# Kernel optimization log

Hardware: AMD Instinct MI355X
Metric: run time of the kernel (lower is better)

## Reference

```python
import jax, jax.numpy as jnp
import numpy as np
from jax import lax

B, T = 16, 64
SD, LD, C, K, A = 256, 256, 32, 32, 6   # state_dim, latent_dim, num_categories, num_classes, action_dim
FS = SD + C * K                          # full_state_dim = 1280
KL_BETA, KL_BAL = 1.0, 0.8


def _conv(x, w, b):  # stride-2, k4, pad1 conv (torch Conv2d(k=4,s=2,p=1))
    y = lax.conv_general_dilated(x, w, (2, 2), ((1, 1), (1, 1)),
                                 dimension_numbers=('NCHW', 'OIHW', 'NCHW'))
    return y + b[None, :, None, None]


def _convT(x, w, b):  # stride-2 VALID conv-transpose: out = (in-1)*2 + k
    y = lax.conv_transpose(x, w, (2, 2), 'VALID',
                           dimension_numbers=('NCHW', 'OIHW', 'NCHW'))
    return y + b[None, :, None, None]


def setup_inputs() -> dict:
    key = jax.random.key(0)
    ks = iter(jax.random.split(key, 64))
    def rn(shape, s=0.05):
        return jax.random.normal(next(ks), shape, jnp.float32) * s
    def zb(n):
        return jnp.zeros((n,), jnp.float32)
    inp = dict(
        observations=jax.random.uniform(next(ks), (B, T + 1, 3, 64, 64), jnp.float32),
        actions=jax.random.randint(next(ks), (B, T), 0, A, dtype=jnp.int32),
        rewards=jax.random.normal(next(ks), (B, T), jnp.float32),
        # encoder: 3->32->64->128->256, then 256*4*4 -> latent_dim
        ew1=rn((32, 3, 4, 4)), eb1=zb(32), ew2=rn((64, 32, 4, 4)), eb2=zb(64),
        ew3=rn((128, 64, 4, 4)), eb3=zb(128), ew4=rn((256, 128, 4, 4)), eb4=zb(256),
        enc_lw=rn((4096, LD)), enc_lb=zb(LD),
        # rssm
        pre_w=rn((C * K + A, SD)), pre_b=zb(SD),
        gru_wi=rn((SD, 3 * SD)), gru_wh=rn((SD, 3 * SD)), gru_bi=zb(3 * SD), gru_bh=zb(3 * SD),
        pri_w1=rn((SD, 256)), pri_b1=zb(256), pri_w2=rn((256, C * K)), pri_b2=zb(C * K),
        post_w1=rn((SD + LD, 256)), post_b1=zb(256), post_w2=rn((256, C * K)), post_b2=zb(C * K),
        # decoder: 1280 -> 1024 -> (1024,1,1) -> 3x64x64
        dec_lw=rn((FS, 1024)), dec_lb=zb(1024),
        dw1=rn((128, 1024, 5, 5)), db1=zb(128), dw2=rn((64, 128, 5, 5)), db2=zb(64),
        dw3=rn((32, 64, 6, 6)), db3=zb(32), dw4=rn((3, 32, 6, 6)), db4=zb(3),
        # reward head
        rw1=rn((FS, 256)), rb1=zb(256), rw2=rn((256, 1)), rb2=zb(1),
        # fixed gumbel noise for straight-through categorical sampling (T,B,C,K)
        gumbel=-jnp.log(-jnp.log(jax.random.uniform(next(ks), (T, B, C, K), jnp.float32, 1e-6, 1.0 - 1e-6))),
    )
    return inp


def reference(observations, actions, rewards,
              ew1, eb1, ew2, eb2, ew3, eb3, ew4, eb4, enc_lw, enc_lb,
              pre_w, pre_b, gru_wi, gru_wh, gru_bi, gru_bh,
              pri_w1, pri_b1, pri_w2, pri_b2, post_w1, post_b1, post_w2, post_b2,
              dec_lw, dec_lb, dw1, db1, dw2, db2, dw3, db3, dw4, db4,
              rw1, rb1, rw2, rb2, gumbel):
    relu, sg = jax.nn.relu, lax.stop_gradient
    b, tp1 = observations.shape[:2]
    t = tp1 - 1

    # ---- encoder over all frames ----
    x = observations.reshape(-1, 3, 64, 64)
    x = relu(_conv(x, ew1, eb1))
    x = relu(_conv(x, ew2, eb2))
    x = relu(_conv(x, ew3, eb3))
    x = relu(_conv(x, ew4, eb4))                      # (B*(T+1), 256, 4, 4)
    embeds = (x.reshape(x.shape[0], -1) @ enc_lw + enc_lb).reshape(b, tp1, LD)

    a_oh = jax.nn.one_hot(actions, A, dtype=jnp.float32).transpose(1, 0, 2)  # (T,B,A)
    emb_t = embeds[:, 1:].transpose(1, 0, 2)                                 # (T,B,LD)

    h0 = jnp.zeros((b, SD), jnp.float32)
    s0 = jnp.zeros((b, C * K), jnp.float32)

    def step(carry, inp):
        h, stoch = carry
        a, e, g = inp
        xin = relu(jnp.concatenate([stoch, a], -1) @ pre_w + pre_b)
        # GRU cell
        gi = xin @ gru_wi + gru_bi
        gh = h @ gru_wh + gru_bh
        ir, iz, inn = jnp.split(gi, 3, -1)
        hr, hz, hn = jnp.split(gh, 3, -1)
        r = jax.nn.sigmoid(ir + hr)
        z = jax.nn.sigmoid(iz + hz)
        n = jnp.tanh(inn + r * hn)
        h = (1.0 - z) * n + z * h
        prior = (relu(h @ pri_w1 + pri_b1) @ pri_w2 + pri_b2).reshape(b, C, K)
        post = (relu(jnp.concatenate([h, e], -1) @ post_w1 + post_b1) @ post_w2 + post_b2).reshape(b, C, K)
        # straight-through categorical sample from posterior
        idx = jnp.argmax(post + g, -1)
        probs = jax.nn.softmax(post, -1)
        sample = jax.nn.one_hot(idx, K, dtype=jnp.float32) + probs - sg(probs)
        stoch = sample.reshape(b, C * K)
        full = jnp.concatenate([h, stoch], -1)
        return (h, stoch), (prior, post, full)

    _, (priors, posts, fulls) = lax.scan(step, (h0, s0), (a_oh, emb_t, gumbel))
    priors = priors.transpose(1, 0, 2, 3)             # (B,T,C,K)
    posts = posts.transpose(1, 0, 2, 3)
    fulls = fulls.transpose(1, 0, 2).reshape(b * t, FS)

    # ---- decoder ----
    d = (fulls @ dec_lw + dec_lb).reshape(-1, 1024, 1, 1)
    d = relu(_convT(d, dw1, db1))                     # (.,128,5,5)
    d = relu(_convT(d, dw2, db2))                     # (.,64,13,13)
    d = relu(_convT(d, dw3, db3))                     # (.,32,30,30)
    recon = _convT(d, dw4, db4).reshape(b, t, 3, 64, 64)

    reward_pred = (relu(fulls @ rw1 + rb1) @ rw2 + rb2).reshape(b, t)

    recon_loss = jnp.mean((recon - observations[:, 1:]) ** 2)
    reward_loss = jnp.mean((reward_pred - rewards) ** 2)

    pp = jax.nn.softmax(posts, -1) + 1e-8
    qp = jax.nn.softmax(priors, -1) + 1e-8
    pl = jnp.log(pp)
    ql = jnp.log(qp)
    kl = (KL_BAL * jnp.mean(jnp.sum(sg(pp) * (sg(pl) - ql), -1))
          + (1.0 - KL_BAL) * jnp.mean(jnp.sum(pp * (pl - sg(ql)), -1)))

    return recon_loss + reward_loss + KL_BETA * kl
```

## Files before the change

### kernel.cpp

```cpp
#include <hip/hip_runtime.h>
#include <math.h>

#define DI __device__ __forceinline__

constexpr int TB = 16, TT = 64, NF = 1040, FSD = 1280;
constexpr int CHF = 208;
constexpr int CHN = 256;

constexpr size_t OFF_X1C  = 0;
constexpr size_t OFF_X2C  = 6815744;
constexpr size_t OFF_X3C  = 10223616;
constexpr size_t OFF_D0T  = 0;
constexpr size_t OFF_DD1  = 262144;
constexpr size_t OFF_DD2  = 1081344;
constexpr size_t OFF_DD3  = 3850240;
constexpr size_t OFF_X4   = 11927552;
constexpr size_t OFF_W1T  = 11927552;
constexpr size_t OFF_W2T  = 15204352;
constexpr size_t OFF_W3T  = 15409152;
constexpr size_t OFF_W4P  = 15482880;
constexpr size_t OFF_EMB  = 16187392;
constexpr size_t OFF_FULL = 16453632;
constexpr size_t OFF_PRI  = 17764352;
constexpr size_t OFF_POS  = 18812928;
constexpr size_t OFF_H    = 19861504;
constexpr size_t OFF_GI   = 19865600;
constexpr size_t OFF_GH   = 19877888;
constexpr size_t OFF_Q1   = 19890176;
constexpr size_t OFF_CIDX = 19894272;
constexpr size_t OFF_BARS = 19894784;
constexpr size_t OFF_ACC  = 19895296;
constexpr size_t WS_NEED_BYTES = (OFF_ACC + 16) * 4;

__global__ void k_init(int* bars, double* accs) {
  int i = threadIdx.x;
  if (i < 512) bars[i] = 0;
  if (i < 4) accs[i] = 0.0;
}

__global__ void __launch_bounds__(256) k_conv1(const float* __restrict__ obs,
    const float* __restrict__ w, const float* __restrict__ b, float* __restrict__ out, int fb) {
  __shared__ float in_s[3*66*66];
  __shared__ float w_s[32*48];
  const int f = blockIdx.x, tid = threadIdx.x;
  const float* src = obs + (size_t)(fb + f)*12288;
  for (int i = tid; i < 3*66*66; i += 256) {
    int c = i/4356, p = i%4356, y = p/66, x = p%66;
    float v = 0.f;
    if (y >= 1 && y <= 64 && x >= 1 && x <= 64) v = src[(c<<12) + ((y-1)<<6) + (x-1)];
    in_s[i] = v;
  }
  for (int i = tid; i < 32*48; i += 256) w_s[i] = w[i];
  __syncthreads();
  for (int pp = 0; pp < 4; ++pp) {
    int pos = tid + pp*256;
    int y = pos >> 5, x = pos & 31;
    float tp[48];
    #pragma unroll
    for (int c = 0; c < 3; ++c)
      #pragma unroll
      for (int ky = 0; ky < 4; ++ky)
        #pragma unroll
        for (int kx = 0; kx < 4; ++kx)
          tp[c*16+ky*4+kx] = in_s[c*4356 + (2*y+ky)*66 + (2*x+kx)];
    for (int o = 0; o < 32; ++o) {
      float acc = b[o];
      #pragma unroll
      for (int t = 0; t < 48; ++t) acc += tp[t]*w_s[o*48+t];
      out[((size_t)f*32 + o)*1024 + pos] = fmaxf(acc, 0.f);
    }
  }
}

__global__ void __launch_bounds__(256) k_conv2(const float* __restrict__ in,
    const float* __restrict__ w, const float* __restrict__ bias, float* __restrict__ out) {
  __shared__ float in_s[8*34*34];
  __shared__ float w_s[32*128];
  const int f = blockIdx.x, oh = blockIdx.y, tid = threadIdx.x;
  const int y = tid >> 4, x = tid & 15;
  float acc[32];
  #pragma unroll
  for (int o = 0; o < 32; ++o) acc[o] = bias[oh*32 + o];
  for (int cc = 0; cc < 4; ++cc) {
    __syncthreads();
    for (int i = tid; i < 8*34*34; i += 256) {
      int c = i/1156, p = i%1156, yy = p/34, xx = p%34;
      float v = 0.f;
      if (yy >= 1 && yy <= 32 && xx >= 1 && xx <= 32)
        v = in[((size_t)f*32 + cc*8 + c)*1024 + ((yy-1)<<5) + (xx-1)];
      in_s[i] = v;
    }
    for (int i = tid; i < 4096; i += 256) {
      int o = i >> 7, r = i & 127;
      w_s[i] = w[(oh*32+o)*512 + cc*128 + r];
    }
    __syncthreads();
    #pragma unroll
    for (int c = 0; c < 8; ++c) {
      float tp[16];
      #pragma unroll
      for (int ky = 0; ky < 4; ++ky)
        #pragma unroll
        for (int kx = 0; kx < 4; ++kx)
          tp[ky*4+kx] = in_s[c*1156 + (2*y+ky)*34 + (2*x+kx)];
      #pragma unroll
      for (int o = 0; o < 32; ++o) {
        float a2 = acc[o];
        #pragma unroll
        for (int t = 0; t < 16; ++t) a2 += tp[t]*w_s[(o<<7) + (c<<4) + t];
        acc[o] = a2;
      }
    }
  }
  #pragma unroll
  for (int o = 0; o < 32; ++o)
    out[((size_t)f*64 + oh*32 + o)*256 + tid] = fmaxf(acc[o], 0.f);
}

__global__ void __launch_bounds__(256) k_conv3(const float* __restrict__ in,
    const float* __restrict__ w, const float* __restrict__ bias, float* __restrict__ out) {
  __shared__ float in_s[4*18*18];
  __shared__ float w_s[128*64];
  const int f = blockIdx.x, tid = threadIdx.x;
  const int pos = tid & 63, cog = tid >> 6;
  const int y = pos >> 3, x = pos & 7;
  float acc[32];
  #pragma unroll
  for (int o = 0; o < 32; ++o) acc[o] = bias[cog*32+o];
  for (int cc = 0; cc < 16; ++cc) {
    __syncthreads();
    for (int i = tid; i < 1296; i += 256) {
      int c = i/324, p = i%324, yy = p/18, xx = p%18;
      float v = 0.f;
      if (yy >= 1 && yy <= 16 && xx >= 1 && xx <= 16)
        v = in[((size_t)f*64 + cc*4 + c)*256 + ((yy-1)<<4) + (xx-1)];
      in_s[i] = v;
    }
    for (int i = tid; i < 8192; i += 256) {
      int o = i >> 6, r = i & 63;
      w_s[i] = w[o*1024 + cc*64 + r];
    }
    __syncthreads();
    #pragma unroll
    for (int c = 0; c < 4; ++c) {
      float tp[16];
      #pragma unroll
      for (int ky = 0; ky < 4; ++ky)
        #pragma unroll
        for (int kx = 0; kx < 4; ++kx)
          tp[ky*4+kx] = in_s[c*324 + (2*y+ky)*18 + (2*x+kx)];
      #pragma unroll
      for (int o = 0; o < 32; ++o) {
        float a2 = acc[o];
        #pragma unroll
        for (int t = 0; t < 16; ++t) a2 += tp[t]*w_s[((cog*32+o)<<6) + (c<<4) + t];
        acc[o] = a2;
      }
    }
  }
  #pragma unroll
  for (int o = 0; o < 32; ++o)
    out[((size_t)f*128 + cog*32 + o)*64 + pos] = fmaxf(acc[o], 0.f);
}

__global__ void __launch_bounds__(256) k_conv4(const float* __restrict__ in,
    const float* __restrict__ w, const float* __restrict__ bias, float* __restrict__ out, int fb) {
  __shared__ float a_s[32*256];
  __shared__ float w_s[64*32];
  const int f0 = blockIdx.x * 16, o0 = blockIdx.y * 64, tid = threadIdx.x;
  const int fl = tid >> 4, pos = tid & 15;
  float acc[64];
  #pragma unroll
  for (int o = 0; o < 64; ++o) acc[o] = 0.f;
  for (int K0 = 0; K0 < 2048; K0 += 32) {
    __syncthreads();
    for (int i = tid; i < 8192; i += 256) {
      int kk = i >> 8, row = i & 255;
      int K = K0 + kk, ci = K >> 4, tap = K & 15;
      int ff = f0 + (row >> 4), pp = row & 15;
      int yy = ((pp >> 2) << 1) + (tap >> 2) - 1;
      int xx = ((pp & 3) << 1) + (tap & 3) - 1;
      float v = 0.f;
      if (yy >= 0 && yy < 8 && xx >= 0 && xx < 8)
        v = in[((size_t)ff*128 + ci)*64 + yy*8 + xx];
      a_s[kk*256 + row] = v;
    }
    for (int i = tid; i < 2048; i += 256) {
      int o = i >> 5, kk = i & 31;
      w_s[i] = w[(o0 + o)*2048 + K0 + kk];
    }
    __syncthreads();
    #pragma unroll
    for (int kk = 0; kk < 32; ++kk) {
      float av = a_s[kk*256 + tid];
      #pragma unroll
      for (int o = 0; o < 64; ++o) acc[o] += av * w_s[o*32 + kk];
    }
  }
  for (int o = 0; o < 64; ++o)
    out[(((size_t)(fb + f0 + fl))*256 + o0+o)*16 + pos] = fmaxf(acc[o] + bias[o0+o], 0.f);
}

__global__ void __launch_bounds__(256) k_enclin(const float* __restrict__ x4,
    const float* __restrict__ w, const float* __restrict__ b, float* __restrict__ emb) {
  __shared__ float a_s[4*1024];
  const int f0 = blockIdx.x*4, tid = threadIdx.x;
  float acc[4] = {0.f,0.f,0.f,0.f};
  for (int K0 = 0; K0 < 4096; K0 += 1024) {
    __syncthreads();
    for (int i = tid; i < 4096; i += 256) {
      int r = i >> 10, k = i & 1023;
      a_s[i] = x4[((size_t)(f0+r))*4096 + K0 + k];
    }
    __syncthreads();
    for (int k = 0; k < 1024; ++k) {
      float wv = w[(K0+k)*256 + tid];
      #pragma unroll
      for (int r = 0; r < 4; ++r) acc[r] += a_s[(r<<10) + k] * wv;
    }
  }
  #pragma unroll
  for (int r = 0; r < 4; ++r) emb[((size_t)(f0+r))*256 + tid] = acc[r] + b[tid];
}

__global__ void k_wtrans(const float* __restrict__ dw1, const float* __restrict__ dw2,
                         const float* __restrict__ dw3, const float* __restrict__ dw4,
                         float* __restrict__ w1t, float* __restrict__ w2t,
                         float* __restrict__ w3t, float* __restrict__ w4p) {
  int i = blockIdx.x*256 + threadIdx.x;
  if (i < 1024*3200) {
    int k = i / 3200, c = i % 3200;
    int o = c / 25, r = c % 25, y = r / 5, x = r % 5;
    w1t[i] = dw1[(o*1024 + k)*25 + (4-y)*5 + (4-x)];
  }
  if (i < 25*128*64) {
    int tap = i / 8192, r = i % 8192, ii = r >> 6, o = r & 63;
    w2t[i] = dw2[(o*128 + ii)*25 + tap];
  }
  if (i < 36*64*32) {
    int tap = i / 2048, r = i % 2048, ii = r >> 5, o = r & 31;
    w3t[i] = dw3[(o*64 + ii)*36 + tap];
  }
  if (i < 4*9*96) {
    int par = i / 864, r = i % 864, d9 = r / 96, q = r % 96, ii = q/3, o = q%3;
    int py = par >> 1, px = par & 1, d2 = d9 / 3, d = d9 % 3;
    int ky = 5 - py - 2*d2, kx = 5 - px - 2*d;
    w4p[i] = dw4[(o*32 + ii)*36 + ky*6 + kx];
  }
}

struct ScanArgs {
  const float *pre_w, *pre_b, *wi, *wh, *bi, *bh, *qw1, *qb1, *qw2, *qb2, *emb, *gum;
  const int* act;
  float *hbuf, *gibuf, *ghbuf, *q1buf, *fulls, *posts;
  int *curidx, *bars;
};

DI void chain_bar(int* bar, int target) {
  __syncthreads();
  if (threadIdx.x == 0) {
    __threadfence();
    __hip_atomic_fetch_add(bar, 1, __ATOMIC_RELEASE, __HIP_MEMORY_SCOPE_AGENT);
    while (__hip_atomic_load(bar, __ATOMIC_ACQUIRE, __HIP_MEMORY_SCOPE_AGENT) < target) {
      __builtin_amdgcn_s_sleep(1);
    }
  }
  __syncthreads();
  __threadfence();
}

__global__ void __launch_bounds__(256) k_scan(ScanArgs a) {
  const int tid = threadIdx.x;
  const int chain = blockIdx.x & 15;
  const int sub = blockIdx.x >> 4;
  __shared__ float xin_s[256], h_s[256], h2_s[256], e_s[256], q1_s[256], red_s[256];
  __shared__ float post_s[64];
  __shared__ int idx_s[2];
  int* bar = a.bars + chain*32;
  int bk = 0;
  float* hb  = a.hbuf  + chain*256;
  float* gib = a.gibuf + chain*768;
  float* ghb = a.ghbuf + chain*768;
  float* q1b = a.q1buf + chain*256;
  int* cidx  = a.curidx + chain*32;

  for (int t = 0; t < TT; ++t) {
    const int row = chain*TT + t;
    h_s[tid] = (t == 0) ? 0.f : hb[tid];
    {
      float v = a.pre_b[tid];
      int act = a.act[chain*TT + t];
      v += a.pre_w[(1024 + act)*256 + tid];
      if (t > 0) {
        #pragma unroll
        for (int c = 0; c < 32; ++c) {
          int ix = cidx[c];
          v += a.pre_w[(c*32 + ix)*256 + tid];
        }
      }
      xin_s[tid] = fmaxf(v, 0.f);
    }
    __syncthreads();
    if (tid < 192) {
      int cl = tid % 96, kp = tid / 96;
      int col = (sub & 7)*96 + cl;
      const float* W   = (sub < 8) ? a.wi : a.wh;
      const float* src = (sub < 8) ? xin_s : h_s;
      const float* wp = W + (size_t)(kp*128)*768 + col;
      const float* sp = src + kp*128;
      float p = 0.f;
      #pragma unroll 8
      for (int k = 0; k < 128; ++k) p += sp[k] * wp[(size_t)k*768];
      red_s[kp*96 + cl] = p;
    }
    __syncthreads();
    if (tid < 96) {
      int col = (sub & 7)*96 + tid;
      float v = red_s[tid] + red_s[96+tid];
      if (sub < 8) gib[col] = v + a.bi[col];
      else         ghb[col] = v + a.bh[col];
    }
    chain_bar(bar, 16*(++bk));
    {
      float gi0 = gib[tid], gi1 = gib[256+tid], gi2 = gib[512+tid];
      float gh0 = ghb[tid], gh1 = ghb[256+tid], gh2 = ghb[512+tid];
      float r = 1.f/(1.f+expf(-(gi0+gh0)));
      float z = 1.f/(1.f+expf(-(gi1+gh1)));
      float nn = tanhf(gi2 + r*gh2);
      float hn = (1.f - z)*nn + z*h_s[tid];
      h2_s[tid] = hn;
      e_s[tid] = a.emb[((size_t)chain*65 + t + 1)*256 + tid];
      if (sub == 0) {
        hb[tid] = hn;
        a.fulls[(size_t)row*FSD + tid] = hn;
      }
    }
    __syncthreads();
    {
      int cl = tid & 15, kp = tid >> 4;
      int col = sub*16 + cl;
      float p = 0.f;
      int k0 = kp*32;
      #pragma unroll 8
      for (int k = 0; k < 32; ++k) {
        int kk = k0 + k;
        float v = (kk < 256) ? h2_s[kk] : e_s[kk-256];
        p += v * a.qw1[(size_t)kk*256 + col];
      }
      red_s[kp*16 + cl] = p;
    }
    __syncthreads();
    if (tid < 16) {
      int col = sub*16 + tid;
      float v = a.qb1[col];
      #pragma unroll
      for (int p = 0; p < 16; ++p) v += red_s[p*16 + tid];
      q1b[col] = fmaxf(v, 0.f);
    }
    chain_bar(bar, 16*(++bk));
    q1_s[tid] = q1b[tid];
    __syncthreads();
    {
      int cl = tid & 63, kp = tid >> 6;
      int col = sub*64 + cl;
      float p = 0.f;
      int k0 = kp*64;
      #pragma unroll 8
      for (int k = 0; k < 64; ++k) p += q1_s[k0+k] * a.qw2[(size_t)(k0+k)*1024 + col];
      red_s[kp*64 + cl] = p;
    }
    __syncthreads();
    if (tid < 64) {
      int col = sub*64 + tid;
      float v = a.qb2[col] + red_s[tid] + red_s[64+tid] + red_s[128+tid] + red_s[192+tid];
      a.posts[(size_t)row*1024 + col] = v;
      post_s[tid] = v;
    }
    __syncthreads();
    if (tid < 2) {
      int cat = sub*2 + tid;
      const float* g = a.gum + (((size_t)t*16 + chain)*32 + cat)*32;
      float best = post_s[tid*32] + g[0]; int bst = 0;
      #pragma unroll
      for (int k = 1; k < 32; ++k) {
        float v = post_s[tid*32 + k] + g[k];
        if (v > best) { best = v; bst = k; }
      }
      idx_s[tid] = bst;
      cidx[cat] = bst;
    }
    __syncthreads();
    if (tid < 64) {
      int k = tid & 31, cl = tid >> 5;
      a.fulls[(size_t)row*FSD + 256 + (sub*2 + cl)*32 + k] = (k == idx_s[cl]) ? 1.f : 0.f;
    }
    chain_bar(bar, 16*(++bk));
  }
}

__global__ void __launch_bounds__(256) k_priors(const float* __restrict__ fulls,
    const float* __restrict__ w1, const float* __restrict__ b1,
    const float* __restrict__ w2, const float* __restrict__ b2, float* __restrict__ priors) {
  __shared__ float h_s[16*256];
  __shared__ float p1_s[16*256];
  const int r0 = blockIdx.x*16, tid = threadIdx.x;
  for (int i = tid; i < 4096; i += 256) {
    int r = i >> 8, k = i & 255;
    h_s[i] = fulls[((size_t)(r0+r))*FSD + k];
  }
  __syncthreads();
  float acc[16];
  #pragma unroll
  for (int r = 0; r < 16; ++r) acc[r] = b1[tid];
  for (int k = 0; k < 256; ++k) {
    float wv = w1[k*256 + tid];
    #pragma unroll
    for (int r = 0; r < 16; ++r) acc[r] += h_s[(r<<8)+k]*wv;
  }
  #pragma unroll
  for (int r = 0; r < 16; ++r) p1_s[(r<<8)+tid] = fmaxf(acc[r], 0.f);
  __syncthreads();
  float a2[16][4];
  #pragma unroll
  for (int r = 0; r < 16; ++r)
    #pragma unroll
    for (int q = 0; q < 4; ++q) a2[r][q] = b2[q*256 + tid];
  for (int k = 0; k < 256; ++k) {
    float w0 = w2[k*1024 + tid], wv1 = w2[k*1024 + 256 + tid];
    float wv2 = w2[k*1024 + 512 + tid], wv3 = w2[k*1024 + 768 + tid];
    #pragma unroll
    for (int r = 0; r < 16; ++r) {
      float pv = p1_s[(r<<8)+k];
      a2[r][0] += pv*w0; a2[r][1] += pv*wv1; a2[r][2] += pv*wv2; a2[r][3] += pv*wv3;
    }
  }
  for (int r = 0; r < 16; ++r)
    #pragma unroll
    for (int q = 0; q < 4; ++q)
      priors[((size_t)(r0+r))*1024 + q*256 + tid] = a2[r][q];
}

__global__ void __launch_bounds__(256) k_declin(const float* __restrict__ fulls,
    const float* __restrict__ w, const float* __restrict__ b, float* __restrict__ d0t, int nb) {
  __shared__ float f_s[32*257];
  __shared__ float w_s[32*32];
  const int k0 = blockIdx.x*32, tid = threadIdx.x;
  float acc[32];
  #pragma unroll
  for (int kt = 0; kt < 32; ++kt) acc[kt] = 0.f;
  for (int K0 = 0; K0 < 1280; K0 += 32) {
    __syncthreads();
    {
      const float4* src = (const float4*)(fulls + ((size_t)(nb+tid))*FSD + K0);
      #pragma unroll
      for (int q = 0; q < 8; ++q) {
        float4 v = src[q];
        f_s[(q*4+0)*257 + tid] = v.x;
        f_s[(q*4+1)*257 + tid] = v.y;
        f_s[(q*4+2)*257 + tid] = v.z;
        f_s[(q*4+3)*257 + tid] = v.w;
      }
    }
    for (int i = tid; i < 1024; i += 256) {
      int kk = i >> 5, kt = i & 31;
      w_s[i] = w[(size_t)(K0+kk)*1024 + k0 + kt];
    }
    __syncthreads();
    #pragma unroll
    for (int kk = 0; kk < 32; ++kk) {
      float hv = f_s[kk*257 + tid];
      #pragma unroll
      for (int kt = 0; kt < 32; ++kt) acc[kt] += hv * w_s[kk*32 + kt];
    }
  }
  for (int kt = 0; kt < 32; ++kt) d0t[((size_t)(k0+kt))*CHN + tid] = acc[kt] + b[k0+kt];
}

__global__ void __launch_bounds__(256) k_ct1(const float* __restrict__ d0t,
    const float* __restrict__ w1t, const float* __restrict__ db1, float* __restrict__ dd1) {
  __shared__ float w_s[32*32];
  const int c0 = blockIdx.x*32, tid = threadIdx.x;
  float acc[32];
  #pragma unroll
  for (int ct = 0; ct < 32; ++ct) acc[ct] = 0.f;
  for (int K0 = 0; K0 < 1024; K0 += 32) {
    __syncthreads();
    for (int i = tid; i < 1024; i += 256) {
      int kk = i >> 5, ct = i & 31;
      w_s[i] = w1t[(size_t)(K0+kk)*3200 + c0 + ct];
    }
    __syncthreads();
    #pragma unroll
    for (int kk = 0; kk < 32; ++kk) {
      float av = d0t[((size_t)(K0+kk))*CHN + tid];
      #pragma unroll
      for (int ct = 0; ct < 32; ++ct) acc[ct] += av * w_s[kk*32 + ct];
    }
  }
  #pragma unroll
  for (int ct = 0; ct < 32; ++ct)
    dd1[((size_t)(c0+ct))*CHN + tid] = fmaxf(acc[ct] + db1[(c0+ct)/25], 0.f);
}

__global__ void __launch_bounds__(256) k_ct2(const float* __restrict__ dd1,
    const float* __restrict__ w2t, const float* __restrict__ db2, float* __restrict__ dd2) {
  __shared__ float w_s[128*32];
  const int pos = blockIdx.x, og = blockIdx.y, tid = threadIdx.x;
  const int y = pos/13, x = pos%13;
  const int nl2 = (tid & 127)*2, oh = tid >> 7;
  float acc[16][2];
  #pragma unroll
  for (int o = 0; o < 16; ++o) { acc[o][0] = 0.f; acc[o][1] = 0.f; }
  for (int ky = 0; ky < 5; ++ky) {
    int ty = y + ky - 4;
    if (ty & 1) continue;
    int iy = ty >> 1;
    if (iy < 0 || iy >= 5) continue;
    for (int kx = 0; kx < 5; ++kx) {
      int tx = x + kx - 4;
      if (tx & 1) continue;
      int ix = tx >> 1;
      if (ix < 0 || ix >= 5) continue;
      int tap = ky*5 + kx;
      __syncthreads();
      for (int i = tid; i < 4096; i += 256)
        w_s[i] = w2t[(size_t)tap*8192 + (i >> 5)*64 + og*32 + (i & 31)];
      __syncthreads();
      #pragma unroll 4
      for (int i = 0; i < 128; ++i) {
        float2 v = *(const float2*)(dd1 + ((size_t)(i*25 + iy*5 + ix))*CHN + nl2);
        #pragma unroll
        for (int o = 0; o < 16; ++o) {
          float wv = w_s[i*32 + oh*16 + o];
          acc[o][0] += v.x*wv; acc[o][1] += v.y*wv;
        }
      }
    }
  }
  for (int o = 0; o < 16; ++o) {
    int oo = og*32 + oh*16 + o;
    float bb = db2[oo];
    float2 r; r.x = fmaxf(acc[o][0]+bb, 0.f); r.y = fmaxf(acc[o][1]+bb, 0.f);
    *(float2*)(dd2 + ((size_t)(oo*169 + pos))*CHN + nl2) = r;
  }
}

__global__ void __launch_bounds__(256) k_ct3(const float* __restrict__ dd2,
    const float* __restrict__ w3t, const float* __restrict__ db3, float* __restrict__ dd3) {
  __shared__ float w_s[64*32];
  const int pos = blockIdx.x, tid = threadIdx.x;
  const int y = pos/30, x = pos%30;
  const int nl2 = (tid & 127)*2, oh = tid >> 7;
  float acc[16][2];
  #pragma unroll
  for (int o = 0; o < 16; ++o) { acc[o][0] = 0.f; acc[o][1] = 0.f; }
  for (int ky = 0; ky < 6; ++ky) {
    int ty = y + ky - 5;
    if (ty & 1) continue;
    int iy = ty >> 1;
    if (iy < 0 || iy >= 13) continue;
    for (int kx = 0; kx < 6; ++kx) {
      int tx = x + kx - 5;
      if (tx & 1) continue;
      int ix = tx >> 1;
      if (ix < 0 || ix >= 13) continue;
      int tap = ky*6 + kx;
      __syncthreads();
      for (int i = tid; i < 2048; i += 256) w_s[i] = w3t[(size_t)tap*2048 + i];
      __syncthreads();
      #pragma unroll 2
      for (int i = 0; i < 64; ++i) {
        float2 v = *(const float2*)(dd2 + ((size_t)(i*169 + iy*13 + ix))*CHN + nl2);
        #pragma unroll
        for (int o = 0; o < 16; ++o) {
          float wv = w_s[i*32 + oh*16 + o];
          acc[o][0] += v.x*wv; acc[o][1] += v.y*wv;
        }
      }
    }
  }
  for (int o = 0; o < 16; ++o) {
    int oo = oh*16 + o;
    float bb = db3[oo];
    float2 r; r.x = fmaxf(acc[o][0]+bb, 0.f); r.y = fmaxf(acc[o][1]+bb, 0.f);
    *(float2*)(dd3 + ((size_t)(oo*900 + pos))*CHN + nl2) = r;
  }
}

__global__ void __launch_bounds__(512) k_ct4loss(const float* __restrict__ dd3,
    const float* __restrict__ w4p, const float* __restrict__ db4,
    const float* __restrict__ obs, double* __restrict__ accRec, int nb) {
  __shared__ float in_s[16*10*6*16];
  __shared__ float redf[8];
  const int tid = threadIdx.x, bx = blockIdx.x;
  const int nbt = bx & 15, xt = (bx >> 4) & 7, yt = bx >> 7;
  const int n0 = nbt*16, Y0 = yt*8, X0 = xt*4;
  const int nl = tid & 15, ppos = tid >> 4;
  const int yl = ppos >> 2, xl = ppos & 3;
  float acc[4][3];
  #pragma unroll
  for (int p = 0; p < 4; ++p) { acc[p][0]=db4[0]; acc[p][1]=db4[1]; acc[p][2]=db4[2]; }
  for (int ch = 0; ch < 2; ++ch) {
    __syncthreads();
    for (int i = tid; i < 15360; i += 512) {
      int n2 = i & 15, r = i >> 4;
      int ix = r % 6, r2 = r / 6, iy = r2 % 10, ii = r2 / 10;
      int gy = Y0 - 2 + iy, gx = X0 - 2 + ix;
      float v = 0.f;
      if (gy >= 0 && gy < 30 && gx >= 0 && gx < 30)
        v = dd3[((size_t)((ch*16 + ii)*900 + gy*30 + gx))*CHN + n0 + n2];
      in_s[i] = v;
    }
    __syncthreads();
    #pragma unroll
    for (int par = 0; par < 4; ++par) {
      #pragma unroll
      for (int d2 = 0; d2 < 3; ++d2) {
        int iy = yl + 2 - d2;
        #pragma unroll
        for (int d = 0; d < 3; ++d) {
          int ix = xl + 2 - d;
          const float* wp = w4p + (par*9 + d2*3 + d)*96 + ch*48;
          #pragma unroll 4
          for (int ii = 0; ii < 16; ++ii) {
            float v = in_s[((ii*10 + iy)*6 + ix)*16 + nl];
            acc[par][0] += v*wp[ii*3+0];
            acc[par][1] += v*wp[ii*3+1];
            acc[par][2] += v*wp[ii*3+2];
          }
        }
      }
    }
  }
  const int n = nb + n0 + nl, b = n >> 6, t = n & 63;
  float lsum = 0.f;
  #pragma unroll
  for (int par = 0; par < 4; ++par) {
    int py = par >> 1, px = par & 1;
    int yy = 2*(Y0 + yl) + py, xx = 2*(X0 + xl) + px;
    const float* ob = obs + (size_t)((b*65 + t + 1)*3)*4096 + yy*64 + xx;
    float d0v = acc[par][0] - ob[0];
    float d1v = acc[par][1] - ob[4096];
    float d2v = acc[par][2] - ob[8192];
    lsum += d0v*d0v + d1v*d1v + d2v*d2v;
  }
  #pragma unroll
  for (int off = 32; off > 0; off >>= 1) lsum += __shfl_down(lsum, off);
  if ((tid & 63) == 0) redf[tid >> 6] = lsum;
  __syncthreads();
  if (tid == 0) {
    float s = 0.f;
    for (int i = 0; i < 8; ++i) s += redf[i];
    atomicAdd(accRec, (double)s);
  }
}

__global__ void __launch_bounds__(256) k_reward(const float* __restrict__ fulls,
    const float* __restrict__ w1, const float* __restrict__ b1,
    const float* __restrict__ w2, const float* __restrict__ b2,
    const float* __restrict__ rew, double* __restrict__ accR) {
  __shared__ float f_s[8*1280];
  __shared__ float h_s[8*256];
  const int r0 = blockIdx.x*8, tid = threadIdx.x;
  for (int i = tid; i < 8*1280; i += 256) f_s[i] = fulls[(size_t)r0*FSD + i];
  __syncthreads();
  float acc[8];
  #pragma unroll
  for (int r = 0; r < 8; ++r) acc[r] = b1[tid];
  for (int k = 0; k < 1280; ++k) {
    float wv = w1[(size_t)k*256 + tid];
    #pragma unroll
    for (int r = 0; r < 8; ++r) acc[r] += f_s[r*1280 + k] * wv;
  }
  #pragma unroll
  for (int r = 0; r < 8; ++r) h_s[(r<<8) + tid] = fmaxf(acc[r], 0.f);
  __syncthreads();
  int r = tid >> 5, l = tid & 31;
  float p = 0.f;
  for (int j = l; j < 256; j += 32) p += h_s[(r<<8) + j] * w2[j];
  #pragma unroll
  for (int off = 16; off > 0; off >>= 1) p += __shfl_down(p, off, 32);
  if (l == 0) {
    float d = p + b2[0] - rew[r0 + r];
    atomicAdd(accR, (double)(d*d));
  }
}

__global__ void __launch_bounds__(256) k_kl(const float* __restrict__ posts,
    const float* __restrict__ priors, double* __restrict__ accK) {
  const int u = blockIdx.x*256 + threadIdx.x;
  const float* po = posts  + (size_t)(u >> 5)*1024 + (u & 31)*32;
  const float* pr = priors + (size_t)(u >> 5)*1024 + (u & 31)*32;
  float pv[32], qv[32];
  float m1 = -1e30f, m2 = -1e30f;
  #pragma unroll
  for (int k = 0; k < 32; ++k) {
    pv[k] = po[k]; m1 = fmaxf(m1, pv[k]);
    qv[k] = pr[k]; m2 = fmaxf(m2, qv[k]);
  }
  float s1 = 0.f, s2 = 0.f;
  #pragma unroll
  for (int k = 0; k < 32; ++k) {
    pv[k] = expf(pv[k]-m1); s1 += pv[k];
    qv[k] = expf(qv[k]-m2); s2 += qv[k];
  }
  float i1 = 1.f/s1, i2 = 1.f/s2;
  float kl = 0.f;
  #pragma unroll
  for (int k = 0; k < 32; ++k) {
    float pp = pv[k]*i1 + 1e-8f;
    float qq = qv[k]*i2 + 1e-8f;
    kl += pp * (logf(pp) - logf(qq));
  }
  #pragma unroll
  for (int off = 32; off > 0; off >>= 1) kl += __shfl_down(kl, off);
  __shared__ float red[4];
  if ((threadIdx.x & 63) == 0) red[threadIdx.x >> 6] = kl;
  __syncthreads();
  if (threadIdx.x == 0) atomicAdd(accK, (double)(red[0]+red[1]+red[2]+red[3]));
}

__global__ void k_fin(const double* __restrict__ accs, float* __restrict__ out) {
  out[0] = (float)(accs[0]/12582912.0 + accs[1]/1024.0 + accs[2]/32768.0);
}

extern "C" void kernel_launch(void* const* d_in, const int* in_sizes, int n_in,
                              void* d_out, int out_size, void* d_ws, size_t ws_size,
                              hipStream_t stream) {
  (void)in_sizes; (void)n_in; (void)out_size;
  if (ws_size < WS_NEED_BYTES) return;
  const float* obs   = (const float*)d_in[0];
  const int*   act   = (const int*)  d_in[1];
  const float* rew   = (const float*)d_in[2];
  const float* ew1   = (const float*)d_in[3];
  const float* eb1   = (const float*)d_in[4];
  const float* ew2   = (const float*)d_in[5];
  const float* eb2   = (const float*)d_in[6];
  const float* ew3   = (const float*)d_in[7];
  const float* eb3   = (const float*)d_in[8];
  const float* ew4   = (const float*)d_in[9];
  const float* eb4   = (const float*)d_in[10];
  const float* enc_lw= (const float*)d_in[11];
  const float* enc_lb= (const float*)d_in[12];
  const float* pre_w = (const float*)d_in[13];
  const float* pre_b = (const float*)d_in[14];
  const float* gru_wi= (const float*)d_in[15];
  const float* gru_wh= (const float*)d_in[16];
  const float* gru_bi= (const float*)d_in[17];
  const float* gru_bh= (const float*)d_in[18];
  const float* pri_w1= (const float*)d_in[19];
  const float* pri_b1= (const float*)d_in[20];
  const float* pri_w2= (const float*)d_in[21];
  const float* pri_b2= (const float*)d_in[22];
  const float* post_w1=(const float*)d_in[23];
  const float* post_b1=(const float*)d_in[24];
  const float* post_w2=(const float*)d_in[25];
  const float* post_b2=(const float*)d_in[26];
  const float* dec_lw= (const float*)d_in[27];
  const float* dec_lb= (const float*)d_in[28];
  const float* dw1   = (const float*)d_in[29];
  const float* db1   = (const float*)d_in[30];
  const float* dw2   = (const float*)d_in[31];
  const float* db2   = (const float*)d_in[32];
  const float* dw3   = (const float*)d_in[33];
  const float* db3   = (const float*)d_in[34];
  const float* dw4   = (const float*)d_in[35];
  const float* db4   = (const float*)d_in[36];
  const float* rw1   = (const float*)d_in[37];
  const float* rb1   = (const float*)d_in[38];
  const float* rw2   = (const float*)d_in[39];
  const float* rb2   = (const float*)d_in[40];
  const float* gum   = (const float*)d_in[41];

  float* ws = (float*)d_ws;
  float* x1c  = ws + OFF_X1C;
  float* x2c  = ws + OFF_X2C;
  float* x3c  = ws + OFF_X3C;
  float* x4   = ws + OFF_X4;
  float* emb  = ws + OFF_EMB;
  float* fulls= ws + OFF_FULL;
  float* priB = ws + OFF_PRI;
  float* posB = ws + OFF_POS;
  float* d0tc = ws + OFF_D0T;
  float* dd1c = ws + OFF_DD1;
  float* dd2c = ws + OFF_DD2;
  float* dd3c = ws + OFF_DD3;
  float* w1t  = ws + OFF_W1T;
  float* w2t  = ws + OFF_W2T;
  float* w3t  = ws + OFF_W3T;
  float* w4p  = ws + OFF_W4P;
  int*   cidx = (int*)(ws + OFF_CIDX);
  int*   bars = (int*)(ws + OFF_BARS);
  double* accs= (double*)(ws + OFF_ACC);

  k_init<<<1, 512, 0, stream>>>(bars, accs);

  for (int fc = 0; fc < 5; ++fc) {
    int fb = fc*CHF;
    k_conv1<<<CHF, 256, 0, stream>>>(obs, ew1, eb1, x1c, fb);
    k_conv2<<<dim3(CHF,2), 256, 0, stream>>>(x1c, ew2, eb2, x2c);
    k_conv3<<<CHF, 256, 0, stream>>>(x2c, ew3, eb3, x3c);
    k_conv4<<<dim3(CHF/16,4), 256, 0, stream>>>(x3c, ew4, eb4, x4, fb);
  }
  k_enclin<<<260, 256, 0, stream>>>(x4, enc_lw, enc_lb, emb);

  ScanArgs sa;
  sa.pre_w = pre_w; sa.pre_b = pre_b;
  sa.wi = gru_wi; sa.wh = gru_wh; sa.bi = gru_bi; sa.bh = gru_bh;
  sa.qw1 = post_w1; sa.qb1 = post_b1; sa.qw2 = post_w2; sa.qb2 = post_b2;
  sa.emb = emb; sa.gum = gum; sa.act = act;
  sa.hbuf = ws + OFF_H; sa.gibuf = ws + OFF_GI; sa.ghbuf = ws + OFF_GH;
  sa.q1buf = ws + OFF_Q1; sa.fulls = fulls; sa.posts = posB;
  sa.curidx = cidx; sa.bars = bars;
  k_scan<<<256, 256, 0, stream>>>(sa);

  k_priors<<<64, 256, 0, stream>>>(fulls, pri_w1, pri_b1, pri_w2, pri_b2, priB);
  k_wtrans<<<12800, 256, 0, stream>>>(dw1, dw2, dw3, dw4, w1t, w2t, w3t, w4p);

  for (int nc = 0; nc < 4; ++nc) {
    int nb = nc*CHN;
    k_declin<<<32, 256, 0, stream>>>(fulls, dec_lw, dec_lb, d0tc, nb);
    k_ct1<<<100, 256, 0, stream>>>(d0tc, w1t, db1, dd1c);
    k_ct2<<<dim3(169,2), 256, 0, stream>>>(dd1c, w2t, db2, dd2c);
    k_ct3<<<900, 256, 0, stream>>>(dd2c, w3t, db3, dd3c);
    k_ct4loss<<<512, 512, 0, stream>>>(dd3c, w4p, db4, obs, accs + 0, nb);
  }

  k_reward<<<128, 256, 0, stream>>>(fulls, rw1, rb1, rw2, rb2, rew, accs + 1);
  k_kl<<<128, 256, 0, stream>>>(posB, priB, accs + 2);
  k_fin<<<1, 1, 0, stream>>>(accs, (float*)d_out);
}
```

Measured before the change: 17.54 ms.

## Run each RSSM scan chain in one 1024-thread block, dropping grid barriers

The recurrent scan used to spread each of the 16 chains over 16 workgroups, synchronised through global atomic spin barriers three times per step with state exchanged via global buffers. Now each chain runs entirely in one 1024-thread workgroup, holding the GRU gates, hidden state, and posterior in shared memory, and picks the argmax with wavefront shuffles. This removes the cross-block barrier latency and the global round trips, but only 16 workgroups are active, so each step's matvecs run on far fewer compute units and weight-bandwidth parallelism drops.

```diff
diff --git a/kernel.cpp b/kernel.cpp
--- a/kernel.cpp
+++ b/kernel.cpp
@@ -23,18 +23,11 @@
 constexpr size_t OFF_FULL = 16453632;
 constexpr size_t OFF_PRI  = 17764352;
 constexpr size_t OFF_POS  = 18812928;
-constexpr size_t OFF_H    = 19861504;
-constexpr size_t OFF_GI   = 19865600;
-constexpr size_t OFF_GH   = 19877888;
-constexpr size_t OFF_Q1   = 19890176;
-constexpr size_t OFF_CIDX = 19894272;
-constexpr size_t OFF_BARS = 19894784;
 constexpr size_t OFF_ACC  = 19895296;
 constexpr size_t WS_NEED_BYTES = (OFF_ACC + 16) * 4;
 
-__global__ void k_init(int* bars, double* accs) {
+__global__ void k_init(double* accs) {
   int i = threadIdx.x;
-  if (i < 512) bars[i] = 0;
   if (i < 4) accs[i] = 0.0;
 }
 
@@ -249,152 +242,107 @@
   }
 }
 
-struct ScanArgs {
+struct Scan2Args {
   const float *pre_w, *pre_b, *wi, *wh, *bi, *bh, *qw1, *qb1, *qw2, *qb2, *emb, *gum;
   const int* act;
-  float *hbuf, *gibuf, *ghbuf, *q1buf, *fulls, *posts;
-  int *curidx, *bars;
+  float *fulls, *posts;
 };
 
-DI void chain_bar(int* bar, int target) {
+__global__ void __launch_bounds__(1024) k_scan2(Scan2Args a) {
+  const int tid = threadIdx.x;
+  const int chain = blockIdx.x;
+  __shared__ float xin_s[256], h_s[256], e_s[256], q1_s[256];
+  __shared__ float gi_s[768], gh_s[768];
+  __shared__ float post_s[1024];
+  __shared__ float red_s[512];
+  __shared__ int cidx_s[32];
+  if (tid < 256) h_s[tid] = 0.f;
   __syncthreads();
-  if (threadIdx.x == 0) {
-    __threadfence();
-    __hip_atomic_fetch_add(bar, 1, __ATOMIC_RELEASE, __HIP_MEMORY_SCOPE_AGENT);
-    while (__hip_atomic_load(bar, __ATOMIC_ACQUIRE, __HIP_MEMORY_SCOPE_AGENT) < target) {
-      __builtin_amdgcn_s_sleep(1);
-    }
-  }
-  __syncthreads();
-  __threadfence();
-}
-
-__global__ void __launch_bounds__(256) k_scan(ScanArgs a) {
-  const int tid = threadIdx.x;
-  const int chain = blockIdx.x & 15;
-  const int sub = blockIdx.x >> 4;
-  __shared__ float xin_s[256], h_s[256], h2_s[256], e_s[256], q1_s[256], red_s[256];
-  __shared__ float post_s[64];
-  __shared__ int idx_s[2];
-  int* bar = a.bars + chain*32;
-  int bk = 0;
-  float* hb  = a.hbuf  + chain*256;
-  float* gib = a.gibuf + chain*768;
-  float* ghb = a.ghbuf + chain*768;
-  float* q1b = a.q1buf + chain*256;
-  int* cidx  = a.curidx + chain*32;
-
   for (int t = 0; t < TT; ++t) {
     const int row = chain*TT + t;
-    h_s[tid] = (t == 0) ? 0.f : hb[tid];
-    {
-      float v = a.pre_b[tid];
+    if (tid < 256) {
+      e_s[tid] = a.emb[((size_t)chain*65 + t + 1)*256 + tid];
+    } else if (tid < 512) {
+      int i = tid - 256;
+      float v = a.pre_b[i];
       int act = a.act[chain*TT + t];
-      v += a.pre_w[(1024 + act)*256 + tid];
+      v += a.pre_w[(size_t)(1024 + act)*256 + i];
       if (t > 0) {
         #pragma unroll
-        for (int c = 0; c < 32; ++c) {
-          int ix = cidx[c];
-          v += a.pre_w[(c*32 + ix)*256 + tid];
-        }
-      }
-      xin_s[tid] = fmaxf(v, 0.f);
-    }
-    __syncthreads();
-    if (tid < 192) {
-      int cl = tid % 96, kp = tid / 96;
-      int col = (sub & 7)*96 + cl;
-      const float* W   = (sub < 8) ? a.wi : a.wh;
-      const float* src = (sub < 8) ? xin_s : h_s;
-      const float* wp = W + (size_t)(kp*128)*768 + col;
-      const float* sp = src + kp*128;
+        for (int c = 0; c < 32; ++c)
+          v += a.pre_w[(size_t)(c*32 + cidx_s[c])*256 + i];
+      }
+      xin_s[i] = fmaxf(v, 0.f);
+    }
+    __syncthreads();
+    if (tid < 768) {
       float p = 0.f;
       #pragma unroll 8
-      for (int k = 0; k < 128; ++k) p += sp[k] * wp[(size_t)k*768];
-      red_s[kp*96 + cl] = p;
-    }
-    __syncthreads();
-    if (tid < 96) {
-      int col = (sub & 7)*96 + tid;
-      float v = red_s[tid] + red_s[96+tid];
-      if (sub < 8) gib[col] = v + a.bi[col];
-      else         ghb[col] = v + a.bh[col];
-    }
-    chain_bar(bar, 16*(++bk));
+      for (int k = 0; k < 256; ++k) p += xin_s[k] * a.wi[(size_t)k*768 + tid];
+      gi_s[tid] = p + a.bi[tid];
+    } else {
+      int c2 = tid - 768;
+      float p = 0.f;
+      #pragma unroll 8
+      for (int k = 0; k < 256; ++k) p += h_s[k] * a.wh[(size_t)k*768 + c2];
+      gh_s[c2] = p + a.bh[c2];
+    }
+    if (tid < 512) {
+      int c2 = 256 + tid;
+      float p = 0.f;
+      #pragma unroll 8
+      for (int k = 0; k < 256; ++k) p += h_s[k] * a.wh[(size_t)k*768 + c2];
+      gh_s[c2] = p + a.bh[c2];
+    }
+    __syncthreads();
+    if (tid < 256) {
+      float rr = 1.f/(1.f+expf(-(gi_s[tid]      + gh_s[tid])));
+      float zz = 1.f/(1.f+expf(-(gi_s[256+tid]  + gh_s[256+tid])));
+      float nn = tanhf(gi_s[512+tid] + rr*gh_s[512+tid]);
+      float hn = (1.f - zz)*nn + zz*h_s[tid];
+      h_s[tid] = hn;
+      a.fulls[(size_t)row*FSD + tid] = hn;
+    }
+    __syncthreads();
+    if (tid < 512) {
+      int col = tid & 255, half = tid >> 8;
+      int k0 = half << 8;
+      float p = 0.f;
+      #pragma unroll 8
+      for (int k2 = 0; k2 < 256; ++k2) {
+        int kk = k0 + k2;
+        float v = (kk < 256) ? h_s[kk] : e_s[kk-256];
+        p += v * a.qw1[(size_t)kk*256 + col];
+      }
+      red_s[tid] = p;
+    }
+    __syncthreads();
+    if (tid < 256) q1_s[tid] = fmaxf(red_s[tid] + red_s[256+tid] + a.qb1[tid], 0.f);
+    __syncthreads();
     {
-      float gi0 = gib[tid], gi1 = gib[256+tid], gi2 = gib[512+tid];
-      float gh0 = ghb[tid], gh1 = ghb[256+tid], gh2 = ghb[512+tid];
-      float r = 1.f/(1.f+expf(-(gi0+gh0)));
-      float z = 1.f/(1.f+expf(-(gi1+gh1)));
-      float nn = tanhf(gi2 + r*gh2);
-      float hn = (1.f - z)*nn + z*h_s[tid];
-      h2_s[tid] = hn;
-      e_s[tid] = a.emb[((size_t)chain*65 + t + 1)*256 + tid];
-      if (sub == 0) {
-        hb[tid] = hn;
-        a.fulls[(size_t)row*FSD + tid] = hn;
-      }
+      float p = 0.f;
+      #pragma unroll 8
+      for (int k = 0; k < 256; ++k) p += q1_s[k] * a.qw2[(size_t)k*1024 + tid];
+      p += a.qb2[tid];
+      post_s[tid] = p;
+      a.posts[(size_t)row*1024 + tid] = p;
     }
     __syncthreads();
     {
-      int cl = tid & 15, kp = tid >> 4;
-      int col = sub*16 + cl;
-      float p = 0.f;
-      int k0 = kp*32;
-      #pragma unroll 8
-      for (int k = 0; k < 32; ++k) {
-        int kk = k0 + k;
-        float v = (kk < 256) ? h2_s[kk] : e_s[kk-256];
-        p += v * a.qw1[(size_t)kk*256 + col];
-      }
-      red_s[kp*16 + cl] = p;
-    }
-    __syncthreads();
-    if (tid < 16) {
-      int col = sub*16 + tid;
-      float v = a.qb1[col];
-      #pragma unroll
-      for (int p = 0; p < 16; ++p) v += red_s[p*16 + tid];
-      q1b[col] = fmaxf(v, 0.f);
-    }
-    chain_bar(bar, 16*(++bk));
-    q1_s[tid] = q1b[tid];
-    __syncthreads();
-    {
-      int cl = tid & 63, kp = tid >> 6;
-      int col = sub*64 + cl;
-      float p = 0.f;
-      int k0 = kp*64;
-      #pragma unroll 8
-      for (int k = 0; k < 64; ++k) p += q1_s[k0+k] * a.qw2[(size_t)(k0+k)*1024 + col];
-      red_s[kp*64 + cl] = p;
-    }
-    __syncthreads();
-    if (tid < 64) {
-      int col = sub*64 + tid;
-      float v = a.qb2[col] + red_s[tid] + red_s[64+tid] + red_s[128+tid] + red_s[192+tid];
-      a.posts[(size_t)row*1024 + col] = v;
-      post_s[tid] = v;
-    }
-    __syncthreads();
-    if (tid < 2) {
-      int cat = sub*2 + tid;
-      const float* g = a.gum + (((size_t)t*16 + chain)*32 + cat)*32;
-      float best = post_s[tid*32] + g[0]; int bst = 0;
-      #pragma unroll
-      for (int k = 1; k < 32; ++k) {
-        float v = post_s[tid*32 + k] + g[k];
-        if (v > best) { best = v; bst = k; }
-      }
-      idx_s[tid] = bst;
-      cidx[cat] = bst;
-    }
-    __syncthreads();
-    if (tid < 64) {
-      int k = tid & 31, cl = tid >> 5;
-      a.fulls[(size_t)row*FSD + 256 + (sub*2 + cl)*32 + k] = (k == idx_s[cl]) ? 1.f : 0.f;
-    }
-    chain_bar(bar, 16*(++bk));
+      int cat = tid >> 5, k = tid & 31;
+      float v = post_s[cat*32 + k] + a.gum[(((size_t)t*16 + chain)*32 + cat)*32 + k];
+      int bidx = k;
+      #pragma unroll
+      for (int off = 16; off > 0; off >>= 1) {
+        float ov = __shfl_down(v, off, 32);
+        int oi = __shfl_down(bidx, off, 32);
+        if (ov > v || (ov == v && oi < bidx)) { v = ov; bidx = oi; }
+      }
+      int best = __shfl(bidx, 0, 32);
+      if (k == 0) cidx_s[cat] = best;
+      a.fulls[(size_t)row*FSD + 256 + tid] = (k == best) ? 1.f : 0.f;
+    }
+    __syncthreads();
   }
 }
 
@@ -789,11 +737,9 @@
   float* w2t  = ws + OFF_W2T;
   float* w3t  = ws + OFF_W3T;
   float* w4p  = ws + OFF_W4P;
-  int*   cidx = (int*)(ws + OFF_CIDX);
-  int*   bars = (int*)(ws + OFF_BARS);
   double* accs= (double*)(ws + OFF_ACC);
 
-  k_init<<<1, 512, 0, stream>>>(bars, accs);
+  k_init<<<1, 64, 0, stream>>>(accs);
 
   for (int fc = 0; fc < 5; ++fc) {
     int fb = fc*CHF;
@@ -804,15 +750,13 @@
   }
   k_enclin<<<260, 256, 0, stream>>>(x4, enc_lw, enc_lb, emb);
 
-  ScanArgs sa;
+  Scan2Args sa;
   sa.pre_w = pre_w; sa.pre_b = pre_b;
   sa.wi = gru_wi; sa.wh = gru_wh; sa.bi = gru_bi; sa.bh = gru_bh;
   sa.qw1 = post_w1; sa.qb1 = post_b1; sa.qw2 = post_w2; sa.qb2 = post_b2;
   sa.emb = emb; sa.gum = gum; sa.act = act;
-  sa.hbuf = ws + OFF_H; sa.gibuf = ws + OFF_GI; sa.ghbuf = ws + OFF_GH;
-  sa.q1buf = ws + OFF_Q1; sa.fulls = fulls; sa.posts = posB;
-  sa.curidx = cidx; sa.bars = bars;
-  k_scan<<<256, 256, 0, stream>>>(sa);
+  sa.fulls = fulls; sa.posts = posB;
+  k_scan2<<<16, 1024, 0, stream>>>(sa);
 
   k_priors<<<64, 256, 0, stream>>>(fulls, pri_w1, pri_b1, pri_w2, pri_b2, priB);
   k_wtrans<<<12800, 256, 0, stream>>>(dw1, dw2, dw3, dw4, w1t, w2t, w3t, w4p);
```

New measurement: 14.31 ms. 1.23x faster.
